# Performance work log

Measured on AMD Instinct MI355X. Metric: run time of the kernel, lower is better.

Reference implementation:

```python
import jax, jax.numpy as jnp
import numpy as np

# UDH_UPPER-style 16-joint upper-body skeleton tree (edge list in topological order)
N = 16
PARENT = [0, 1, 2, 3, 4, 3, 6, 7, 8, 9, 3, 11, 12, 13, 14]
CHILD = [1, 2, 3, 4, 5, 6, 7, 8, 9, 10, 11, 12, 13, 14, 15]
BATCH = 262144


def rotation_6d_to_matrix(d6):
    """Zhou et al. 6d -> 3x3 rotation. d6: [..., 6] -> [..., 3, 3] (rows b1,b2,b3)."""
    a1, a2 = d6[..., :3], d6[..., 3:]
    b1 = a1 / jnp.linalg.norm(a1, axis=-1, keepdims=True)
    b2 = a2 - jnp.sum(b1 * a2, axis=-1, keepdims=True) * b1
    b2 = b2 / jnp.linalg.norm(b2, axis=-1, keepdims=True)
    b3 = jnp.cross(b1, b2)
    return jnp.stack((b1, b2, b3), axis=-2)


def setup_inputs() -> dict:
    key = jax.random.key(0)
    k1, k2 = jax.random.split(key)
    angles = jax.random.normal(k1, (BATCH, N, 6), dtype=jnp.float32)
    # reference skeleton landmark positions (buffer self.xyz), shape [1, N, 3]
    xyz = jax.random.normal(k2, (1, N, 3), dtype=jnp.float32)
    return {"angles": angles, "xyz": xyz}


def reference(angles, xyz):
    """Skeleton.points: 6d angles -> world-space joint XYZ, shape [B, N, 3].

    Faithful to _rotation2points: M[c] = M[p] @ m(rot_c, xyz_c - xyz_p),
    where m packs (r, r @ t) into a rigid transform; we track the rigid
    transform as (R_world [B,3,3], p_world [B,3]) instead of 4x4 matrices.
    """
    R = rotation_6d_to_matrix(angles)  # [B, N, 3, 3]
    ref = xyz[0]                       # [N, 3]
    Rw = [None] * N
    pw = [None] * N
    # root: M[0] = m(rot[:,0], xyz[:,0])
    Rw[0] = R[:, 0]
    pw[0] = jnp.einsum('bij,j->bi', R[:, 0], ref[0])
    for p, c in zip(PARENT, CHILD):
        t = ref[c] - ref[p]                              # [3] bone offset
        local_t = jnp.einsum('bij,j->bi', R[:, c], t)    # r @ t
        Rw[c] = jnp.einsum('bij,bjk->bik', Rw[p], R[:, c])
        pw[c] = jnp.einsum('bij,bj->bi', Rw[p], local_t) + pw[p]
    return jnp.stack(pw, axis=1)  # [B, N, 3] == stack(M)[..., :3, 3]
```

## Files before the change

### kernel.cpp

```cpp
#include <hip/hip_runtime.h>


namespace {

constexpr int NJ = 16;

__device__ __forceinline__ void rot6d(const float* __restrict__ a, float R[9]) {
    float inv1 = rsqrtf(a[0]*a[0] + a[1]*a[1] + a[2]*a[2]);
    float b10 = a[0]*inv1, b11 = a[1]*inv1, b12 = a[2]*inv1;
    float d = b10*a[3] + b11*a[4] + b12*a[5];
    float c0 = a[3] - d*b10, c1 = a[4] - d*b11, c2 = a[5] - d*b12;
    float inv2 = rsqrtf(c0*c0 + c1*c1 + c2*c2);
    float b20 = c0*inv2, b21 = c1*inv2, b22 = c2*inv2;
    R[0] = b10; R[1] = b11; R[2] = b12;
    R[3] = b20; R[4] = b21; R[5] = b22;
    R[6] = b11*b22 - b12*b21;
    R[7] = b12*b20 - b10*b22;
    R[8] = b10*b21 - b11*b20;
}

__global__ __launch_bounds__(256) void skel_kernel(
    const float* __restrict__ angles,
    const float* __restrict__ xyz,
    float* __restrict__ out,
    int batch)
{
    const int b = blockIdx.x * 256 + threadIdx.x;
    if (b >= batch) return;

    const float4* a4 = (const float4*)(angles + (size_t)b * (NJ * 6));
    float4 v[24];
#pragma unroll
    for (int k = 0; k < 24; ++k) v[k] = a4[k];

    __builtin_amdgcn_sched_barrier(0);

    float af[NJ * 6];
#pragma unroll
    for (int k = 0; k < 24; ++k) {
        af[4*k + 0] = v[k].x; af[4*k + 1] = v[k].y;
        af[4*k + 2] = v[k].z; af[4*k + 3] = v[k].w;
    }

    float* ob = out + (size_t)b * (NJ * 3);

    float R[9], Rw[9], pw[3], Rw3[9], pw3[3];

    rot6d(&af[0], Rw);
    {
        float x = xyz[0], y = xyz[1], z = xyz[2];
        pw[0] = Rw[0]*x + Rw[1]*y + Rw[2]*z;
        pw[1] = Rw[3]*x + Rw[4]*y + Rw[5]*z;
        pw[2] = Rw[6]*x + Rw[7]*y + Rw[8]*z;
    }
    ob[0] = pw[0]; ob[1] = pw[1]; ob[2] = pw[2];

    constexpr int PAR[15] = {0, 1, 2, 3, 4, 3, 6, 7, 8, 9, 3, 11, 12, 13, 14};

#pragma unroll
    for (int e = 0; e < 15; ++e) {
        const int c = e + 1;
        const int p = PAR[e];

        if (p == 3) {
#pragma unroll
            for (int k = 0; k < 9; ++k) Rw[k] = Rw3[k];
            pw[0] = pw3[0]; pw[1] = pw3[1]; pw[2] = pw3[2];
        }

        rot6d(&af[c * 6], R);

        float tx = xyz[c * 3 + 0] - xyz[p * 3 + 0];
        float ty = xyz[c * 3 + 1] - xyz[p * 3 + 1];
        float tz = xyz[c * 3 + 2] - xyz[p * 3 + 2];

        float lt0 = R[0]*tx + R[1]*ty + R[2]*tz;
        float lt1 = R[3]*tx + R[4]*ty + R[5]*tz;
        float lt2 = R[6]*tx + R[7]*ty + R[8]*tz;

        float np0 = Rw[0]*lt0 + Rw[1]*lt1 + Rw[2]*lt2 + pw[0];
        float np1 = Rw[3]*lt0 + Rw[4]*lt1 + Rw[5]*lt2 + pw[1];
        float np2 = Rw[6]*lt0 + Rw[7]*lt1 + Rw[8]*lt2 + pw[2];

        float T[9];
#pragma unroll
        for (int i = 0; i < 3; ++i)
#pragma unroll
            for (int j = 0; j < 3; ++j)
                T[i*3 + j] = Rw[i*3 + 0]*R[0*3 + j]
                           + Rw[i*3 + 1]*R[1*3 + j]
                           + Rw[i*3 + 2]*R[2*3 + j];
#pragma unroll
        for (int k = 0; k < 9; ++k) Rw[k] = T[k];
        pw[0] = np0; pw[1] = np1; pw[2] = np2;

        ob[c*3 + 0] = np0; ob[c*3 + 1] = np1; ob[c*3 + 2] = np2;

        if (c == 3) {
#pragma unroll
            for (int k = 0; k < 9; ++k) Rw3[k] = Rw[k];
            pw3[0] = pw[0]; pw3[1] = pw[1]; pw3[2] = pw[2];
        }
    }
}

}

extern "C" void kernel_launch(void* const* d_in, const int* in_sizes, int n_in,
                              void* d_out, int out_size, void* d_ws, size_t ws_size,
                              hipStream_t stream) {
    const float* angles = (const float*)d_in[0];
    const float* xyz    = (const float*)d_in[1];
    float* out          = (float*)d_out;

    const int batch = in_sizes[0] / (NJ * 6);
    dim3 grid((batch + 255) / 256);
    skel_kernel<<<grid, 256, 0, stream>>>(angles, xyz, out, batch);
}
```

Baseline: 176.2 us.

## Stage angle loads and output stores through LDS for coalesced access

Replaces per-thread strided float4 loads of 384 bytes and scalar output stores with cooperative coalesced loads into a padded LDS tile. Each thread then reads its own slice from LDS, and results are staged back through LDS for coalesced float4 stores. Work is split into two halves (joints 0-7, then 8-15) so the second half's global loads are issued before the first half's compute. This adds barriers, LDS traffic and a 64-thread block size, which may reduce occupancy flexibility.

```diff
diff --git a/kernel.cpp b/kernel.cpp
--- a/kernel.cpp
+++ b/kernel.cpp
@@ -4,8 +4,9 @@
 namespace {
 
 constexpr int NJ = 16;
+constexpr int SLOT = 13;
 
-__device__ __forceinline__ void rot6d(const float* __restrict__ a, float R[9]) {
+__device__ __forceinline__ void rot6d(const float a[6], float R[9]) {
     float inv1 = rsqrtf(a[0]*a[0] + a[1]*a[1] + a[2]*a[2]);
     float b10 = a[0]*inv1, b11 = a[1]*inv1, b12 = a[2]*inv1;
     float d = b10*a[3] + b11*a[4] + b12*a[5];
@@ -19,88 +20,163 @@
     R[8] = b10*b21 - b11*b20;
 }
 
-__global__ __launch_bounds__(256) void skel_kernel(
+__device__ __forceinline__ void chain_step(const float R[9],
+                                           float tx, float ty, float tz,
+                                           float Rw[9], float pw[3]) {
+    float lt0 = R[0]*tx + R[1]*ty + R[2]*tz;
+    float lt1 = R[3]*tx + R[4]*ty + R[5]*tz;
+    float lt2 = R[6]*tx + R[7]*ty + R[8]*tz;
+    float np0 = Rw[0]*lt0 + Rw[1]*lt1 + Rw[2]*lt2 + pw[0];
+    float np1 = Rw[3]*lt0 + Rw[4]*lt1 + Rw[5]*lt2 + pw[1];
+    float np2 = Rw[6]*lt0 + Rw[7]*lt1 + Rw[8]*lt2 + pw[2];
+    float T[9];
+#pragma unroll
+    for (int i = 0; i < 3; ++i)
+#pragma unroll
+        for (int j = 0; j < 3; ++j)
+            T[i*3 + j] = Rw[i*3 + 0]*R[0*3 + j]
+                       + Rw[i*3 + 1]*R[1*3 + j]
+                       + Rw[i*3 + 2]*R[2*3 + j];
+#pragma unroll
+    for (int k = 0; k < 9; ++k) Rw[k] = T[k];
+    pw[0] = np0; pw[1] = np1; pw[2] = np2;
+}
+
+__global__ __launch_bounds__(64) void skel_kernel(
     const float* __restrict__ angles,
     const float* __restrict__ xyz,
     float* __restrict__ out,
     int batch)
 {
-    const int b = blockIdx.x * 256 + threadIdx.x;
-    if (b >= batch) return;
+    __shared__ float4 W[64 * SLOT];
 
-    const float4* a4 = (const float4*)(angles + (size_t)b * (NJ * 6));
-    float4 v[24];
+    const int lane      = threadIdx.x;
+    const int blockElem = blockIdx.x * 64;
+    const int clampHi   = batch - 1;
+
+    const float4* ang4 = (const float4*)angles;
+    float4*       out4 = (float4*)out;
+
+    float4 vA[12];
 #pragma unroll
-    for (int k = 0; k < 24; ++k) v[k] = a4[k];
-
-    __builtin_amdgcn_sched_barrier(0);
-
-    float af[NJ * 6];
+    for (int j = 0; j < 12; ++j) {
+        int flat = 64 * j + lane;
+        int le = flat / 12, lc = flat % 12;
+        int ge = min(blockElem + le, clampHi);
+        vA[j] = ang4[(size_t)ge * 24 + lc];
+    }
 #pragma unroll
-    for (int k = 0; k < 24; ++k) {
-        af[4*k + 0] = v[k].x; af[4*k + 1] = v[k].y;
-        af[4*k + 2] = v[k].z; af[4*k + 3] = v[k].w;
+    for (int j = 0; j < 12; ++j) {
+        int flat = 64 * j + lane;
+        int le = flat / 12, lc = flat % 12;
+        W[le * SLOT + lc] = vA[j];
     }
 
-    float* ob = out + (size_t)b * (NJ * 3);
+    float4 vB[12];
+#pragma unroll
+    for (int j = 0; j < 12; ++j) {
+        int flat = 64 * j + lane;
+        int le = flat / 12, lc = flat % 12;
+        int ge = min(blockElem + le, clampHi);
+        vB[j] = ang4[(size_t)ge * 24 + 12 + lc];
+    }
+    __builtin_amdgcn_sched_barrier(0);
+    __syncthreads();
 
-    float R[9], Rw[9], pw[3], Rw3[9], pw3[3];
+    float*  slot  = (float*)&W[lane * SLOT];
+    float2* slot2 = (float2*)slot;
 
-    rot6d(&af[0], Rw);
+    float Rw[9], pw[3], Rw3[9], pw3[3], R[9], a[6];
+
+    auto read6 = [&](int jj, float* aa) {
+        float2 x = slot2[3*jj + 0], y = slot2[3*jj + 1], z = slot2[3*jj + 2];
+        aa[0] = x.x; aa[1] = x.y; aa[2] = y.x; aa[3] = y.y; aa[4] = z.x; aa[5] = z.y;
+    };
+    auto write3 = [&](int jj) {
+        slot[3*jj + 0] = pw[0]; slot[3*jj + 1] = pw[1]; slot[3*jj + 2] = pw[2];
+    };
+    auto tvec = [&](int c, int p, float& tx, float& ty, float& tz) {
+        tx = xyz[c*3 + 0] - xyz[p*3 + 0];
+        ty = xyz[c*3 + 1] - xyz[p*3 + 1];
+        tz = xyz[c*3 + 2] - xyz[p*3 + 2];
+    };
+
+    read6(0, a);
+    rot6d(a, Rw);
     {
         float x = xyz[0], y = xyz[1], z = xyz[2];
         pw[0] = Rw[0]*x + Rw[1]*y + Rw[2]*z;
         pw[1] = Rw[3]*x + Rw[4]*y + Rw[5]*z;
         pw[2] = Rw[6]*x + Rw[7]*y + Rw[8]*z;
     }
-    ob[0] = pw[0]; ob[1] = pw[1]; ob[2] = pw[2];
+    write3(0);
 
-    constexpr int PAR[15] = {0, 1, 2, 3, 4, 3, 6, 7, 8, 9, 3, 11, 12, 13, 14};
-
+    constexpr int PA[7] = {0, 1, 2, 3, 4, 3, 6};
 #pragma unroll
-    for (int e = 0; e < 15; ++e) {
-        const int c = e + 1;
-        const int p = PAR[e];
-
+    for (int e = 0; e < 7; ++e) {
+        const int c = e + 1, p = PA[e];
         if (p == 3) {
 #pragma unroll
             for (int k = 0; k < 9; ++k) Rw[k] = Rw3[k];
             pw[0] = pw3[0]; pw[1] = pw3[1]; pw[2] = pw3[2];
         }
-
-        rot6d(&af[c * 6], R);
-
-        float tx = xyz[c * 3 + 0] - xyz[p * 3 + 0];
-        float ty = xyz[c * 3 + 1] - xyz[p * 3 + 1];
-        float tz = xyz[c * 3 + 2] - xyz[p * 3 + 2];
-
-        float lt0 = R[0]*tx + R[1]*ty + R[2]*tz;
-        float lt1 = R[3]*tx + R[4]*ty + R[5]*tz;
-        float lt2 = R[6]*tx + R[7]*ty + R[8]*tz;
-
-        float np0 = Rw[0]*lt0 + Rw[1]*lt1 + Rw[2]*lt2 + pw[0];
-        float np1 = Rw[3]*lt0 + Rw[4]*lt1 + Rw[5]*lt2 + pw[1];
-        float np2 = Rw[6]*lt0 + Rw[7]*lt1 + Rw[8]*lt2 + pw[2];
-
-        float T[9];
-#pragma unroll
-        for (int i = 0; i < 3; ++i)
-#pragma unroll
-            for (int j = 0; j < 3; ++j)
-                T[i*3 + j] = Rw[i*3 + 0]*R[0*3 + j]
-                           + Rw[i*3 + 1]*R[1*3 + j]
-                           + Rw[i*3 + 2]*R[2*3 + j];
-#pragma unroll
-        for (int k = 0; k < 9; ++k) Rw[k] = T[k];
-        pw[0] = np0; pw[1] = np1; pw[2] = np2;
-
-        ob[c*3 + 0] = np0; ob[c*3 + 1] = np1; ob[c*3 + 2] = np2;
-
+        read6(c, a);
+        rot6d(a, R);
+        float tx, ty, tz; tvec(c, p, tx, ty, tz);
+        chain_step(R, tx, ty, tz, Rw, pw);
+        write3(c);
         if (c == 3) {
 #pragma unroll
             for (int k = 0; k < 9; ++k) Rw3[k] = Rw[k];
             pw3[0] = pw[0]; pw3[1] = pw[1]; pw3[2] = pw[2];
         }
+    }
+
+    __syncthreads();
+#pragma unroll
+    for (int j = 0; j < 6; ++j) {
+        int flat = 64 * j + lane;
+        int le = flat / 6, lc = flat % 6;
+        int ge = blockElem + le;
+        const float* sp = (const float*)&W[le * SLOT];
+        float4 v = *(const float4*)(sp + 4 * lc);
+        if (ge < batch) out4[(size_t)ge * 12 + lc] = v;
+    }
+    __syncthreads();
+
+#pragma unroll
+    for (int j = 0; j < 12; ++j) {
+        int flat = 64 * j + lane;
+        int le = flat / 12, lc = flat % 12;
+        W[le * SLOT + lc] = vB[j];
+    }
+    __syncthreads();
+
+    constexpr int PB[8] = {7, 8, 9, 3, 11, 12, 13, 14};
+#pragma unroll
+    for (int e = 0; e < 8; ++e) {
+        const int c = e + 8, p = PB[e];
+        if (p == 3) {
+#pragma unroll
+            for (int k = 0; k < 9; ++k) Rw[k] = Rw3[k];
+            pw[0] = pw3[0]; pw[1] = pw3[1]; pw[2] = pw3[2];
+        }
+        read6(e, a);
+        rot6d(a, R);
+        float tx, ty, tz; tvec(c, p, tx, ty, tz);
+        chain_step(R, tx, ty, tz, Rw, pw);
+        write3(e);
+    }
+
+    __syncthreads();
+#pragma unroll
+    for (int j = 0; j < 6; ++j) {
+        int flat = 64 * j + lane;
+        int le = flat / 6, lc = flat % 6;
+        int ge = blockElem + le;
+        const float* sp = (const float*)&W[le * SLOT];
+        float4 v = *(const float4*)(sp + 4 * lc);
+        if (ge < batch) out4[(size_t)ge * 12 + 6 + lc] = v;
     }
 }
 
@@ -114,6 +190,6 @@
     float* out          = (float*)d_out;
 
     const int batch = in_sizes[0] / (NJ * 6);
-    dim3 grid((batch + 255) / 256);
-    skel_kernel<<<grid, 256, 0, stream>>>(angles, xyz, out, batch);
+    dim3 grid((batch + 63) / 64);
+    skel_kernel<<<grid, 64, 0, stream>>>(angles, xyz, out, batch);
 }
```

New measurement: 199.5 us. 1.13x slower.
